# Optimization experiments

Measured on AMD Instinct MI355X. Metric: run time of the kernel, lower is better.

Reference implementation:

```python
import jax, jax.numpy as jnp
import numpy as np

N_NODES = 100000
N_EDGES = 1600000
IN_FEATS = 256
OUT_FEATS = 128


def setup_inputs() -> dict:
    key = jax.random.key(0)
    k1, k2, k3, k4 = jax.random.split(key, 4)
    feat = jax.random.normal(k1, (N_NODES, IN_FEATS), dtype=jnp.float32)
    # Glorot-uniform-like weight
    limit = np.sqrt(6.0 / (IN_FEATS + OUT_FEATS)).astype(np.float32)
    weight = jax.random.uniform(k2, (IN_FEATS, OUT_FEATS), dtype=jnp.float32,
                                minval=-limit, maxval=limit)
    bias = jnp.zeros((OUT_FEATS,), dtype=jnp.float32)
    src = jax.random.randint(k3, (N_EDGES,), 0, N_NODES, dtype=jnp.int32)
    dst = jax.random.randint(k4, (N_EDGES,), 0, N_NODES, dtype=jnp.int32)
    return {"feat": feat, "weight": weight, "bias": bias, "src": src, "dst": dst}


def reference(feat, weight, bias, src, dst):
    n = feat.shape[0]
    # in-degree per node (edges point src -> dst), clipped to >= 1
    deg = jax.ops.segment_sum(jnp.ones_like(dst, dtype=feat.dtype), dst,
                              num_segments=n)
    norm = jnp.clip(deg, 1.0, None) ** -0.5          # [N]
    norm = norm[:, None]                             # [N, 1]
    h = feat * norm                                  # src-side normalization
    # in_feats > out_feats: project first, then aggregate (cheaper messages)
    h = h @ weight                                   # [N, out]
    agg = jax.ops.segment_sum(h[src], dst, num_segments=n)  # sparse sum-aggregate
    rst = agg * norm + bias                          # dst-side norm + bias
    return rst
```

## Files before the change

### kernel.cpp

```cpp
#include <hip/hip_runtime.h>
#include <hip/hip_bf16.h>

#define IN_F 256
#define OUT_F 128
#define BSH 7
#define BNODES 128
#define MAXBUCK 1024
#define BIN1A_BLOCKS 256
#define BIN1B_BLOCKS 256
#define GEMM_BLOCKS 256
#define BM 32

typedef short bf16x8 __attribute__((ext_vector_type(8)));
typedef float f32x4 __attribute__((ext_vector_type(4)));
typedef unsigned short us8 __attribute__((ext_vector_type(8)));

__device__ __forceinline__ unsigned short f2bf(float x) {
    union { __hip_bfloat16 b; unsigned short u; } cv;
    cv.b = __float2bfloat16(x);
    return cv.u;
}
__device__ inline float bf2f(unsigned short x) {
    union { unsigned u; float f; } v; v.u = ((unsigned)x) << 16;
    return v.f;
}

__device__ __forceinline__ void gload_lds16(const void* g, void* l) {
    __builtin_amdgcn_global_load_lds(
        (const __attribute__((address_space(1))) unsigned int*)g,
        (__attribute__((address_space(3))) unsigned int*)l,
        16, 0, 0);
}

__global__ __launch_bounds__(256) void prep_kernel(const float* __restrict__ W,
                                                   unsigned short* __restrict__ Wt,
                                                   const int* __restrict__ dst,
                                                   int* __restrict__ bhist,
                                                   int n_edges, int nbuck) {
    if ((int)blockIdx.x < BIN1A_BLOCKS) {
        __shared__ int hist[MAXBUCK];
        const int tid = threadIdx.x;
        const int chunk = (n_edges + BIN1A_BLOCKS - 1) / BIN1A_BLOCKS;
        const int lo = blockIdx.x * chunk;
        const int hi = min(lo + chunk, n_edges);

        for (int i = tid; i < MAXBUCK; i += 256) hist[i] = 0;
        __syncthreads();
        for (int e = lo + tid; e < hi; e += 256)
            atomicAdd(&hist[dst[e] >> BSH], 1);
        __syncthreads();
        for (int i = tid; i < nbuck; i += 256) {
            int c = hist[i];
            if (c) atomicAdd(&bhist[i], c);
        }
    } else {
        int n = blockIdx.x - BIN1A_BLOCKS;
        int k = threadIdx.x;
        Wt[n * IN_F + k] = f2bf(W[k * OUT_F + n]);
    }
}

__global__ __launch_bounds__(1024) void bin1b_kernel(const int* __restrict__ src,
                                                     const int* __restrict__ dst,
                                                     const int* __restrict__ bhist,
                                                     int* __restrict__ gcur0,
                                                     unsigned* __restrict__ ebuf,
                                                     int n_edges, int nbuck) {
    __shared__ int scanv[MAXBUCK];
    __shared__ int hist[MAXBUCK];
    __shared__ int lbase[MAXBUCK];
    const int tid = threadIdx.x;
    const int chunk = (n_edges + BIN1B_BLOCKS - 1) / BIN1B_BLOCKS;
    const int lo = blockIdx.x * chunk;
    const int hi = min(lo + chunk, n_edges);

    int own = (tid < nbuck) ? bhist[tid] : 0;
    scanv[tid] = own;
    __syncthreads();
    #pragma unroll
    for (int off = 1; off < MAXBUCK; off <<= 1) {
        int t = (tid >= off) ? scanv[tid - off] : 0;
        __syncthreads();
        scanv[tid] += t;
        __syncthreads();
    }
    int bstart_t = scanv[tid] - own;
    __syncthreads();
    scanv[tid] = bstart_t;
    hist[tid] = 0;
    __syncthreads();

    for (int e = lo + tid; e < hi; e += 1024)
        atomicAdd(&hist[dst[e] >> BSH], 1);
    __syncthreads();
    if (tid < nbuck) {
        int c = hist[tid];
        lbase[tid] = (c > 0) ? (scanv[tid] + atomicAdd(&gcur0[tid], c)) : 0;
        hist[tid] = 0;
    }
    __syncthreads();
    for (int e = lo + tid; e < hi; e += 1024) {
        int d = dst[e];
        int bkt = d >> BSH;
        int off = atomicAdd(&hist[bkt], 1);
        ebuf[lbase[bkt] + off] = ((unsigned)src[e] << BSH) | (unsigned)(d & (BNODES - 1));
    }
}

__global__ __launch_bounds__(1024) void gemm_mfma(const float* __restrict__ feat,
                                                  const unsigned short* __restrict__ Wt,
                                                  unsigned short* __restrict__ h,
                                                  int n_nodes) {
    __shared__ float As[2][BM * IN_F];
    __shared__ unsigned short Bs[OUT_F * IN_F];

    const int tid  = threadIdx.x;
    const int wave = tid >> 6;
    const int lane = tid & 63;
    const int q    = lane >> 4;
    const int rr   = lane & 15;
    const int rowgrp = wave & 1;
    const int colgrp = wave >> 1;

    const int ntiles = (n_nodes + BM - 1) / BM;

    #pragma unroll
    for (int m = 0; m < 4; ++m) {
        int p   = m * 16 + wave;
        int row = 2 * p + (lane >> 5);
        int ch  = lane & 31;
        gload_lds16(Wt + (size_t)row * IN_F + ((ch ^ (row & 7)) * 8),
                    &Bs[p * 2 * IN_F]);
    }

    int t = blockIdx.x;
    if (t < ntiles) {
        const int R0 = t * BM;
        #pragma unroll
        for (int i = 0; i < 2; ++i) {
            int r  = i * 16 + wave;
            int rg = R0 + r; if (rg >= n_nodes) rg = n_nodes - 1;
            gload_lds16(feat + (size_t)rg * IN_F + ((lane ^ (r & 7)) * 4),
                        &As[0][r * IN_F]);
        }
    }
    __syncthreads();

    int buf = 0;
    for (; t < ntiles; t += GEMM_BLOCKS) {
        const int tn = t + GEMM_BLOCKS;
        if (tn < ntiles) {
            const int R0n = tn * BM;
            #pragma unroll
            for (int i = 0; i < 2; ++i) {
                int r  = i * 16 + wave;
                int rg = R0n + r; if (rg >= n_nodes) rg = n_nodes - 1;
                gload_lds16(feat + (size_t)rg * IN_F + ((lane ^ (r & 7)) * 4),
                            &As[buf ^ 1][r * IN_F]);
            }
        }

        f32x4 acc = (f32x4){0.f, 0.f, 0.f, 0.f};

        const int arow = rowgrp * 16 + rr;
        const int brow = colgrp * 16 + rr;
        const f32x4* ap = reinterpret_cast<const f32x4*>(&As[buf][arow * IN_F]);
        const bf16x8* bsv = reinterpret_cast<const bf16x8*>(Bs);

        #pragma unroll
        for (int k0 = 0; k0 < 8; ++k0) {
            f32x4 a0 = ap[(k0 * 8 + 2 * q)     ^ (rr & 7)];
            f32x4 a1 = ap[(k0 * 8 + 2 * q + 1) ^ (rr & 7)];
            bf16x8 afr;
            afr[0] = (short)f2bf(a0[0]);
            afr[1] = (short)f2bf(a0[1]);
            afr[2] = (short)f2bf(a0[2]);
            afr[3] = (short)f2bf(a0[3]);
            afr[4] = (short)f2bf(a1[0]);
            afr[5] = (short)f2bf(a1[1]);
            afr[6] = (short)f2bf(a1[2]);
            afr[7] = (short)f2bf(a1[3]);
            bf16x8 bfr = bsv[brow * 32 + ((k0 * 4 + q) ^ (brow & 7))];
            acc = __builtin_amdgcn_mfma_f32_16x16x32_bf16(afr, bfr, acc, 0, 0, 0);
        }

        __syncthreads();

        const int orow0 = t * BM + rowgrp * 16 + q * 4;
        const int col   = colgrp * 16 + rr;
        #pragma unroll
        for (int j = 0; j < 4; ++j) {
            int orow = orow0 + j;
            if (orow < n_nodes)
                h[(size_t)orow * OUT_F + col] = f2bf(acc[j]);
        }
        buf ^= 1;
    }
}

__global__ __launch_bounds__(256) void bin2_kernel(const unsigned* __restrict__ ebuf,
                                                   const int* __restrict__ bhist,
                                                   int* __restrict__ rstart,
                                                   float* __restrict__ norm,
                                                   int* __restrict__ eidx,
                                                   int n_nodes, int nbuck) {
    __shared__ int bs[MAXBUCK];
    __shared__ int lcnt[BNODES];
    __shared__ int lex[BNODES];
    __shared__ int sh[256];
    const int tid = threadIdx.x;
    const int node0 = blockIdx.x << BSH;

    {
        int v[4], s = 0;
        #pragma unroll
        for (int j = 0; j < 4; ++j) {
            int idx = tid * 4 + j;
            v[j] = (idx < nbuck) ? bhist[idx] : 0;
            s += v[j];
        }
        sh[tid] = s;
        __syncthreads();
        #pragma unroll
        for (int off = 1; off < 256; off <<= 1) {
            int t = (tid >= off) ? sh[tid - off] : 0;
            __syncthreads();
            sh[tid] += t;
            __syncthreads();
        }
        int ex = sh[tid] - s;
        #pragma unroll
        for (int j = 0; j < 4; ++j) {
            bs[tid * 4 + j] = ex;
            ex += v[j];
        }
    }
    __syncthreads();

    const int e0 = bs[blockIdx.x];
    const int e1 = e0 + bhist[blockIdx.x];

    if (tid < BNODES) lcnt[tid] = 0;
    __syncthreads();
    for (int e = e0 + tid; e < e1; e += 256)
        atomicAdd(&lcnt[ebuf[e] & (BNODES - 1)], 1);
    __syncthreads();

    int own = (tid < BNODES) ? lcnt[tid] : 0;
    if (tid < BNODES) lex[tid] = own;
    __syncthreads();
    #pragma unroll
    for (int off = 1; off < BNODES; off <<= 1) {
        int t = (tid >= off && tid < BNODES) ? lex[tid - off] : 0;
        __syncthreads();
        if (tid < BNODES) lex[tid] += t;
        __syncthreads();
    }
    if (tid < BNODES) {
        int ex = lex[tid] - own;
        lex[tid] = ex;
        int g = node0 + tid;
        if (g <= n_nodes) rstart[g] = e0 + ex;
        if (g < n_nodes) {
            float d = (float)own;
            if (d < 1.0f) d = 1.0f;
            norm[g] = 1.0f / sqrtf(d);
        }
        lcnt[tid] = 0;
    }
    __syncthreads();

    for (int e = e0 + tid; e < e1; e += 256) {
        unsigned pk = ebuf[e];
        int dl = pk & (BNODES - 1);
        int pos = atomicAdd(&lcnt[dl], 1);
        eidx[e0 + lex[dl] + pos] = (int)(pk >> BSH);
    }
}

__global__ __launch_bounds__(256) void agg_kernel(const unsigned short* __restrict__ h,
                                                  const int* __restrict__ eidx,
                                                  const int* __restrict__ rstart,
                                                  const float* __restrict__ norm,
                                                  const float* __restrict__ bias,
                                                  float* __restrict__ out,
                                                  int n_nodes) {
    const int wave = threadIdx.x >> 6;
    const int lane = threadIdx.x & 63;
    const int grp  = lane >> 4;
    const int gl   = lane & 15;
    const int node = blockIdx.x * 4 + wave;
    if (node >= n_nodes) return;

    const int start = rstart[node];
    const int cnt   = rstart[node + 1] - start;
    const unsigned short* __restrict__ hb = h + gl * 8;

    float acc[8] = {0.f, 0.f, 0.f, 0.f, 0.f, 0.f, 0.f, 0.f};

    for (int base = 0; base < cnt; base += 64) {
        const int rem = min(64, cnt - base);
        int   ev = (lane < rem) ? eidx[start + base + lane] : 0;
        float nv = (lane < rem) ? norm[ev] : 0.f;

        int j = 0;
        for (; j + 16 <= rem; j += 16) {
            int   s0 = __shfl(ev, j + grp);
            int   s1 = __shfl(ev, j + grp + 4);
            int   s2 = __shfl(ev, j + grp + 8);
            int   s3 = __shfl(ev, j + grp + 12);
            float n0 = __shfl(nv, j + grp);
            float n1 = __shfl(nv, j + grp + 4);
            float n2 = __shfl(nv, j + grp + 8);
            float n3 = __shfl(nv, j + grp + 12);
            us8 v0 = *reinterpret_cast<const us8*>(hb + (size_t)s0 * OUT_F);
            us8 v1 = *reinterpret_cast<const us8*>(hb + (size_t)s1 * OUT_F);
            us8 v2 = *reinterpret_cast<const us8*>(hb + (size_t)s2 * OUT_F);
            us8 v3 = *reinterpret_cast<const us8*>(hb + (size_t)s3 * OUT_F);
            #pragma unroll
            for (int qq = 0; qq < 8; ++qq) {
                acc[qq] += bf2f(v0[qq]) * n0 + bf2f(v1[qq]) * n1
                         + bf2f(v2[qq]) * n2 + bf2f(v3[qq]) * n3;
            }
        }
        for (; j < rem; j += 4) {
            int   je = j + grp;
            int   jc = min(je, rem - 1);
            int   s  = __shfl(ev, jc);
            float nm = __shfl(nv, jc);
            if (je >= rem) nm = 0.f;
            us8 v = *reinterpret_cast<const us8*>(hb + (size_t)s * OUT_F);
            #pragma unroll
            for (int qq = 0; qq < 8; ++qq)
                acc[qq] += bf2f(v[qq]) * nm;
        }
    }

    #pragma unroll
    for (int qq = 0; qq < 8; ++qq) {
        acc[qq] += __shfl_xor(acc[qq], 16);
        acc[qq] += __shfl_xor(acc[qq], 32);
    }

    if (grp == 0) {
        const float nd = norm[node];
        const float4 b0 = *reinterpret_cast<const float4*>(bias + gl * 8);
        const float4 b1 = *reinterpret_cast<const float4*>(bias + gl * 8 + 4);
        float4 r0, r1;
        r0.x = acc[0] * nd + b0.x;
        r0.y = acc[1] * nd + b0.y;
        r0.z = acc[2] * nd + b0.z;
        r0.w = acc[3] * nd + b0.w;
        r1.x = acc[4] * nd + b1.x;
        r1.y = acc[5] * nd + b1.y;
        r1.z = acc[6] * nd + b1.z;
        r1.w = acc[7] * nd + b1.w;
        float* o = out + (size_t)node * OUT_F + gl * 8;
        *reinterpret_cast<float4*>(o)     = r0;
        *reinterpret_cast<float4*>(o + 4) = r1;
    }
}

extern "C" void kernel_launch(void* const* d_in, const int* in_sizes, int n_in,
                              void* d_out, int out_size, void* d_ws, size_t ws_size,
                              hipStream_t stream) {
    const float* feat   = (const float*)d_in[0];
    const float* weight = (const float*)d_in[1];
    const float* bias   = (const float*)d_in[2];
    const int*   src    = (const int*)d_in[3];
    const int*   dst    = (const int*)d_in[4];
    float* out = (float*)d_out;

    const int n_nodes = in_sizes[0] / IN_F;
    const int n_edges = in_sizes[3];
    const int nbuck   = (n_nodes + BNODES - 1) >> BSH;

    char* ws = (char*)d_ws;
    size_t off = 0;
    auto alloc = [&](size_t bytes) {
        char* p = ws + off;
        off += (bytes + 15) & ~(size_t)15;
        return p;
    };
    unsigned short* h  = (unsigned short*)alloc((size_t)n_nodes * OUT_F * 2);
    float* norm        = (float*)alloc((size_t)n_nodes * 4);
    int*   rstart      = (int*)alloc(((size_t)n_nodes + 1) * 4);
    int*   bhist       = (int*)alloc(2 * MAXBUCK * 4);
    int*   gcur0       = bhist + MAXBUCK;
    unsigned short* Wt = (unsigned short*)alloc((size_t)OUT_F * IN_F * 2);
    unsigned* ebuf     = (unsigned*)alloc((size_t)n_edges * 4);
    int*   eidx        = (int*)alloc((size_t)n_edges * 4);

    hipMemsetAsync(bhist, 0, 2 * MAXBUCK * sizeof(int), stream);
    prep_kernel<<<BIN1A_BLOCKS + OUT_F, 256, 0, stream>>>(weight, Wt, dst, bhist,
                                                          n_edges, nbuck);
    gemm_mfma<<<GEMM_BLOCKS, 1024, 0, stream>>>(feat, Wt, h, n_nodes);
    bin1b_kernel<<<BIN1B_BLOCKS, 1024, 0, stream>>>(src, dst, bhist, gcur0,
                                                    ebuf, n_edges, nbuck);
    bin2_kernel<<<nbuck, 256, 0, stream>>>(ebuf, bhist, rstart, norm, eidx,
                                           n_nodes, nbuck);
    agg_kernel<<<(n_nodes + 3) / 4, 256, 0, stream>>>(h, eidx, rstart, norm, bias, out, n_nodes);
}
```

Before: 150.6 us.

## Triple-buffer GEMM feature loads and reuse per-block bucket histograms in binning

The GEMM kernel moves from double to triple buffering of feature tiles in LDS. It uses explicit vmcnt waits and a single barrier per iteration instead of two __syncthreads, and drops the row bounds check by padding the h buffer. The first binning pass now stores each block's bucket histogram to global memory, so the second pass reads it instead of re-scanning dst and recounting. This relies on BIN1A_BLOCKS equal to BIN1B_BLOCKS with identical edge chunking, and the hand-tuned vmcnt counts are fragile.

```diff
diff --git a/kernel.cpp b/kernel.cpp
--- a/kernel.cpp
+++ b/kernel.cpp
@@ -36,6 +36,7 @@
                                                    unsigned short* __restrict__ Wt,
                                                    const int* __restrict__ dst,
                                                    int* __restrict__ bhist,
+                                                   int* __restrict__ perbhist,
                                                    int n_edges, int nbuck) {
     if ((int)blockIdx.x < BIN1A_BLOCKS) {
         __shared__ int hist[MAXBUCK];
@@ -49,8 +50,10 @@
         for (int e = lo + tid; e < hi; e += 256)
             atomicAdd(&hist[dst[e] >> BSH], 1);
         __syncthreads();
+        int* myrow = perbhist + (size_t)blockIdx.x * MAXBUCK;
         for (int i = tid; i < nbuck; i += 256) {
             int c = hist[i];
+            myrow[i] = c;
             if (c) atomicAdd(&bhist[i], c);
         }
     } else {
@@ -63,6 +66,7 @@
 __global__ __launch_bounds__(1024) void bin1b_kernel(const int* __restrict__ src,
                                                      const int* __restrict__ dst,
                                                      const int* __restrict__ bhist,
+                                                     const int* __restrict__ perbhist,
                                                      int* __restrict__ gcur0,
                                                      unsigned* __restrict__ ebuf,
                                                      int n_edges, int nbuck) {
@@ -87,14 +91,10 @@
     int bstart_t = scanv[tid] - own;
     __syncthreads();
     scanv[tid] = bstart_t;
-    hist[tid] = 0;
-    __syncthreads();
-
-    for (int e = lo + tid; e < hi; e += 1024)
-        atomicAdd(&hist[dst[e] >> BSH], 1);
-    __syncthreads();
+    __syncthreads();
+
     if (tid < nbuck) {
-        int c = hist[tid];
+        int c = perbhist[(size_t)blockIdx.x * MAXBUCK + tid];
         lbase[tid] = (c > 0) ? (scanv[tid] + atomicAdd(&gcur0[tid], c)) : 0;
         hist[tid] = 0;
     }
@@ -111,7 +111,7 @@
                                                   const unsigned short* __restrict__ Wt,
                                                   unsigned short* __restrict__ h,
                                                   int n_nodes) {
-    __shared__ float As[2][BM * IN_F];
+    __shared__ float As[3][BM * IN_F];
     __shared__ unsigned short Bs[OUT_F * IN_F];
 
     const int tid  = threadIdx.x;
@@ -123,6 +123,8 @@
     const int colgrp = wave >> 1;
 
     const int ntiles = (n_nodes + BM - 1) / BM;
+    const int nit = ((int)blockIdx.x < ntiles)
+                  ? ((ntiles - (int)blockIdx.x + GEMM_BLOCKS - 1) / GEMM_BLOCKS) : 0;
 
     #pragma unroll
     for (int m = 0; m < 4; ++m) {
@@ -132,41 +134,47 @@
         gload_lds16(Wt + (size_t)row * IN_F + ((ch ^ (row & 7)) * 8),
                     &Bs[p * 2 * IN_F]);
     }
-
-    int t = blockIdx.x;
-    if (t < ntiles) {
-        const int R0 = t * BM;
-        #pragma unroll
-        for (int i = 0; i < 2; ++i) {
-            int r  = i * 16 + wave;
-            int rg = R0 + r; if (rg >= n_nodes) rg = n_nodes - 1;
-            gload_lds16(feat + (size_t)rg * IN_F + ((lane ^ (r & 7)) * 4),
-                        &As[0][r * IN_F]);
-        }
-    }
-    __syncthreads();
-
-    int buf = 0;
-    for (; t < ntiles; t += GEMM_BLOCKS) {
-        const int tn = t + GEMM_BLOCKS;
-        if (tn < ntiles) {
-            const int R0n = tn * BM;
+    #pragma unroll
+    for (int pb = 0; pb < 2; ++pb) {
+        if (pb < nit) {
+            const int R0 = ((int)blockIdx.x + pb * GEMM_BLOCKS) * BM;
             #pragma unroll
-            for (int i = 0; i < 2; ++i) {
-                int r  = i * 16 + wave;
+            for (int ii = 0; ii < 2; ++ii) {
+                int r  = ii * 16 + wave;
+                int rg = R0 + r; if (rg >= n_nodes) rg = n_nodes - 1;
+                gload_lds16(feat + (size_t)rg * IN_F + ((lane ^ (r & 7)) * 4),
+                            &As[pb][r * IN_F]);
+            }
+        }
+    }
+
+    const bf16x8* bsv = reinterpret_cast<const bf16x8*>(Bs);
+    const int arow = rowgrp * 16 + rr;
+    const int brow = colgrp * 16 + rr;
+
+    int t = (int)blockIdx.x;
+    for (int i = 0; i < nit; ++i, t += GEMM_BLOCKS) {
+        if (nit < 4)          asm volatile("s_waitcnt vmcnt(0)" ::: "memory");
+        else if (i == 0)      asm volatile("s_waitcnt vmcnt(2)" ::: "memory");
+        else if (i == 1)      asm volatile("s_waitcnt vmcnt(6)" ::: "memory");
+        else if (i < nit - 1) asm volatile("s_waitcnt vmcnt(10)" ::: "memory");
+        else                  asm volatile("s_waitcnt vmcnt(8)" ::: "memory");
+        __builtin_amdgcn_s_barrier();
+
+        if (i + 2 < nit) {
+            const int R0n = (t + 2 * GEMM_BLOCKS) * BM;
+            float* dbuf = As[(i + 2) % 3];
+            #pragma unroll
+            for (int ii = 0; ii < 2; ++ii) {
+                int r  = ii * 16 + wave;
                 int rg = R0n + r; if (rg >= n_nodes) rg = n_nodes - 1;
                 gload_lds16(feat + (size_t)rg * IN_F + ((lane ^ (r & 7)) * 4),
-                            &As[buf ^ 1][r * IN_F]);
+                            &dbuf[r * IN_F]);
             }
         }
 
         f32x4 acc = (f32x4){0.f, 0.f, 0.f, 0.f};
-
-        const int arow = rowgrp * 16 + rr;
-        const int brow = colgrp * 16 + rr;
-        const f32x4* ap = reinterpret_cast<const f32x4*>(&As[buf][arow * IN_F]);
-        const bf16x8* bsv = reinterpret_cast<const bf16x8*>(Bs);
-
+        const f32x4* ap = reinterpret_cast<const f32x4*>(&As[i % 3][arow * IN_F]);
         #pragma unroll
         for (int k0 = 0; k0 < 8; ++k0) {
             f32x4 a0 = ap[(k0 * 8 + 2 * q)     ^ (rr & 7)];
@@ -184,17 +192,11 @@
             acc = __builtin_amdgcn_mfma_f32_16x16x32_bf16(afr, bfr, acc, 0, 0, 0);
         }
 
-        __syncthreads();
-
         const int orow0 = t * BM + rowgrp * 16 + q * 4;
         const int col   = colgrp * 16 + rr;
         #pragma unroll
-        for (int j = 0; j < 4; ++j) {
-            int orow = orow0 + j;
-            if (orow < n_nodes)
-                h[(size_t)orow * OUT_F + col] = f2bf(acc[j]);
-        }
-        buf ^= 1;
+        for (int j = 0; j < 4; ++j)
+            h[(size_t)(orow0 + j) * OUT_F + col] = f2bf(acc[j]);
     }
 }
 
@@ -382,21 +384,22 @@
         off += (bytes + 15) & ~(size_t)15;
         return p;
     };
-    unsigned short* h  = (unsigned short*)alloc((size_t)n_nodes * OUT_F * 2);
+    unsigned short* h  = (unsigned short*)alloc((size_t)(n_nodes + BM) * OUT_F * 2);
     float* norm        = (float*)alloc((size_t)n_nodes * 4);
     int*   rstart      = (int*)alloc(((size_t)n_nodes + 1) * 4);
     int*   bhist       = (int*)alloc(2 * MAXBUCK * 4);
     int*   gcur0       = bhist + MAXBUCK;
+    int*   perbhist    = (int*)alloc((size_t)BIN1A_BLOCKS * MAXBUCK * 4);
     unsigned short* Wt = (unsigned short*)alloc((size_t)OUT_F * IN_F * 2);
     unsigned* ebuf     = (unsigned*)alloc((size_t)n_edges * 4);
     int*   eidx        = (int*)alloc((size_t)n_edges * 4);
 
     hipMemsetAsync(bhist, 0, 2 * MAXBUCK * sizeof(int), stream);
     prep_kernel<<<BIN1A_BLOCKS + OUT_F, 256, 0, stream>>>(weight, Wt, dst, bhist,
-                                                          n_edges, nbuck);
+                                                          perbhist, n_edges, nbuck);
     gemm_mfma<<<GEMM_BLOCKS, 1024, 0, stream>>>(feat, Wt, h, n_nodes);
-    bin1b_kernel<<<BIN1B_BLOCKS, 1024, 0, stream>>>(src, dst, bhist, gcur0,
-                                                    ebuf, n_edges, nbuck);
+    bin1b_kernel<<<BIN1B_BLOCKS, 1024, 0, stream>>>(src, dst, bhist, perbhist,
+                                                    gcur0, ebuf, n_edges, nbuck);
     bin2_kernel<<<nbuck, 256, 0, stream>>>(ebuf, bhist, rstart, norm, eidx,
                                            n_nodes, nbuck);
     agg_kernel<<<(n_nodes + 3) / 4, 256, 0, stream>>>(h, eidx, rstart, norm, bias, out, n_nodes);
```

New measurement: 149.5 us. No clear change (-0.8%).
